# Kernel tuning notes

Hardware: AMD Instinct MI355X
Metric: run time of the kernel (lower is better)

Reference implementation:

```python
import jax, jax.numpy as jnp
import numpy as np

ALPHA = 0.2          # LeakyReLU negative slope
NEG_INF = -9e15      # mask value from the original code


def setup_inputs() -> dict:
    key = jax.random.key(0)
    k1, k2, k3, k4 = jax.random.split(key, 4)
    B, N, F_in, F_out = 8, 2048, 64, 64
    x = jax.random.normal(k1, (B, N, F_in), dtype=jnp.float32)
    adj = jax.random.randint(k2, (B, N, N), 0, 2, dtype=jnp.int32)
    W = jax.random.normal(k3, (F_in, F_out), dtype=jnp.float32)
    a = jax.random.normal(k4, (2 * F_out, 1), dtype=jnp.float32)
    return {"x": x, "adj": adj, "W": W, "a": a}


def reference(x, adj, W, a):
    # h: [B, N, F_out]
    h = jnp.matmul(x, W)
    F_out = W.shape[1]
    a1 = a[:F_out, 0]   # source half of attention vector
    a2 = a[F_out:, 0]   # target half
    # e_ij = leakyrelu(h_i . a1 + h_j . a2)  -- identical math to the
    # original cat([h_i, h_j]) @ a without materializing [B,N*N,2F].
    s1 = jnp.einsum('bnf,f->bn', h, a1)  # [B, N]
    s2 = jnp.einsum('bnf,f->bn', h, a2)  # [B, N]
    e = jax.nn.leaky_relu(s1[:, :, None] + s2[:, None, :], negative_slope=ALPHA)
    masked = jnp.where(adj > 0, e, NEG_INF)
    attention = jax.nn.softmax(masked, axis=2)  # [B, N, N]
    # dropout p=0.0 / eval mode -> identity
    h_prime = jnp.matmul(attention, h)          # [B, N, F_out]
    return jax.nn.elu(h_prime)                  # concat=True branch
```

## Files before the change

### kernel.cpp

```cpp
#include <hip/hip_runtime.h>
#include <cstdint>

#define LRELU_ALPHA 0.2f
#define NEG_INF -9000000000000000.0f
#define L2E 1.4426950408889634f

typedef __bf16 bf16x8 __attribute__((ext_vector_type(8)));
typedef float floatx4 __attribute__((ext_vector_type(4)));
typedef unsigned int uintx4 __attribute__((ext_vector_type(4)));

constexpr int Bb = 8, Nn = 2048, Ff = 64;
constexpr int TJ = 64;
constexpr int SEGW = 8;
constexpr int SLICE = Nn / SEGW;
constexpr int NT = SLICE / TJ;
constexpr int NROWS = Bb * Nn;
constexpr int MCH = Nn / 64;

__device__ __forceinline__ unsigned short f2bf(float f) {
    unsigned u = __builtin_bit_cast(unsigned, f);
    u = u + 0x7FFFu + ((u >> 16) & 1u);
    return (unsigned short)(u >> 16);
}

__device__ __forceinline__ unsigned cvt_pk_bf16(float lo, float hi) {
    unsigned r;
    asm("v_cvt_pk_bf16_f32 %0, %1, %2" : "=v"(r) : "v"(lo), "v"(hi));
    return r;
}

__global__ __launch_bounds__(256) void gat_prep(
    const float* __restrict__ x, const float* __restrict__ W, const float* __restrict__ a,
    unsigned short* __restrict__ hT, float* __restrict__ s1g, float* __restrict__ s2g)
{
    constexpr int STR2 = 36;
    __shared__ unsigned short hblk[64 * STR2];
    const int tid = threadIdx.x;
    const int blk = blockIdx.x;
    const int b  = blk >> 6;
    const int i0 = (blk & 63) * 32;
    const int w    = tid >> 6;
    const int lane = tid & 63;

    float wcol[64];
    #pragma unroll
    for (int k = 0; k < 64; ++k) wcol[k] = W[k * 64 + lane];
    const float a1 = a[lane], a2 = a[64 + lane];

    for (int r = 0; r < 8; ++r) {
        const int il = w * 8 + r;
        const int i  = i0 + il;
        const float* xrow = x + ((size_t)(b * Nn + i)) * 64;
        float h0 = 0.f, h1 = 0.f, h2 = 0.f, h3 = 0.f;
        #pragma unroll
        for (int k = 0; k < 64; k += 4) {
            h0 = fmaf(xrow[k],     wcol[k],     h0);
            h1 = fmaf(xrow[k + 1], wcol[k + 1], h1);
            h2 = fmaf(xrow[k + 2], wcol[k + 2], h2);
            h3 = fmaf(xrow[k + 3], wcol[k + 3], h3);
        }
        const float h = (h0 + h1) + (h2 + h3);
        float p1 = h * a1, p2 = h * a2;
        #pragma unroll
        for (int off = 32; off; off >>= 1) {
            p1 += __shfl_xor(p1, off);
            p2 += __shfl_xor(p2, off);
        }
        if (lane == 0) { s1g[b * Nn + i] = p1; s2g[b * Nn + i] = p2; }
        hblk[lane * STR2 + il] = f2bf(h);
    }
    __syncthreads();
    {
        const int f = tid >> 2, c = (tid & 3) * 8;
        uint4 v = *reinterpret_cast<const uint4*>(&hblk[f * STR2 + c]);
        *reinterpret_cast<uint4*>(hT + ((size_t)b * 64 + f) * Nn + i0 + c) = v;
    }
}

__global__ __launch_bounds__(512, 4) void gat_attn(
    const int* __restrict__ adj, const unsigned short* __restrict__ hT,
    const float* __restrict__ s1g, const float* __restrict__ s2g,
    float* __restrict__ out)
{
    __shared__ unsigned long long mk_lds[16][33];
    __shared__ float smax_lds[SEGW];
    __shared__ float O_lds[SEGW][16][65];
    __shared__ float l_lds[SEGW][16];

    const int tid  = threadIdx.x;
    const int blk  = blockIdx.x;
    const int b    = blk >> 7;
    const int i0   = (blk & 127) * 16;
    const int s    = tid >> 6;
    const int lane = tid & 63;
    const int fl   = lane & 15;
    const int q    = lane >> 4;

    {
        const float4 v = *reinterpret_cast<const float4*>(&s2g[b * Nn + s * SLICE + lane * 4]);
        float sm = fmaxf(fmaxf(v.x, v.y), fmaxf(v.z, v.w));
        #pragma unroll
        for (int off = 32; off; off >>= 1) sm = fmaxf(sm, __shfl_xor(sm, off));
        if (lane == 0) smax_lds[s] = sm;
    }

    #pragma unroll
    for (int rr = 0; rr < 2; ++rr) {
        const int rloc = s * 2 + rr;
        const int* ar = adj + ((size_t)(b * Nn + i0 + rloc)) * Nn;
        unsigned long long acc = 0;
        #pragma unroll
        for (int cb = 0; cb < MCH; ++cb) {
            const int v = ar[cb * 64 + lane];
            const unsigned long long mb = __ballot(v > 0);
            if (lane == cb) acc = mb;
        }
        if (lane < 32) mk_lds[rloc][lane] = acc;
    }

    const int i = i0 + fl;
    const float s1v = s1g[b * Nn + i];
    const unsigned short* hTb = hT + (size_t)b * 64 * Nn + s * SLICE;
    const float* s2b = s2g + b * Nn + s * SLICE;

    __syncthreads();

    float s2mx = smax_lds[0];
    #pragma unroll
    for (int k = 1; k < SEGW; ++k) s2mx = fmaxf(s2mx, smax_lds[k]);
    float mub = s1v + s2mx;
    mub = fmaxf(mub, LRELU_ALPHA * mub);
    const float ci = -mub * L2E;

    float l = 0.f;
    floatx4 C[4] = {};

    #pragma unroll
    for (int jt = 0; jt < NT; ++jt) {
        const int jloc = jt * TJ;

        const unsigned long long mk = mk_lds[fl][s * NT + jt];
        const float4 sA = *reinterpret_cast<const float4*>(&s2b[jloc + q * 8]);
        const float4 sB = *reinterpret_cast<const float4*>(&s2b[jloc + q * 8 + 4]);
        const float4 sC = *reinterpret_cast<const float4*>(&s2b[jloc + 32 + q * 8]);
        const float4 sD = *reinterpret_cast<const float4*>(&s2b[jloc + 32 + q * 8 + 4]);

        bf16x8 Bv[8];
        #pragma unroll
        for (int u = 0; u < 4; ++u) {
            Bv[2 * u] = *reinterpret_cast<const bf16x8*>(
                hTb + (size_t)(u * 16 + fl) * Nn + jloc + q * 8);
            Bv[2 * u + 1] = *reinterpret_cast<const bf16x8*>(
                hTb + (size_t)(u * 16 + fl) * Nn + jloc + 32 + q * 8);
        }

        const unsigned blo = ((unsigned)(mk >> (q * 8))) & 0xFFu;
        const unsigned bhi = ((unsigned)(mk >> (32 + q * 8))) & 0xFFu;

        float p[16];
        {
            const float s2v0[8] = { sA.x, sA.y, sA.z, sA.w, sB.x, sB.y, sB.z, sB.w };
            const float s2v1[8] = { sC.x, sC.y, sC.z, sC.w, sD.x, sD.y, sD.z, sD.w };
            #pragma unroll
            for (int jj = 0; jj < 8; ++jj) {
                float ev = s1v + s2v0[jj];
                ev = fmaxf(ev, LRELU_ALPHA * ev);
                const float t = exp2f(fmaf(ev, L2E, ci));
                p[jj] = (blo & (1u << jj)) ? t : 0.f;
                l += p[jj];
            }
            #pragma unroll
            for (int jj = 0; jj < 8; ++jj) {
                float ev = s1v + s2v1[jj];
                ev = fmaxf(ev, LRELU_ALPHA * ev);
                const float t = exp2f(fmaf(ev, L2E, ci));
                p[8 + jj] = (bhi & (1u << jj)) ? t : 0.f;
                l += p[8 + jj];
            }
        }

        uintx4 pa, pb;
        #pragma unroll
        for (int d = 0; d < 4; ++d) {
            pa[d] = cvt_pk_bf16(p[2 * d],     p[2 * d + 1]);
            pb[d] = cvt_pk_bf16(p[8 + 2 * d], p[8 + 2 * d + 1]);
        }
        const bf16x8 A0 = __builtin_bit_cast(bf16x8, pa);
        const bf16x8 A1 = __builtin_bit_cast(bf16x8, pb);

        __builtin_amdgcn_s_setprio(1);
        #pragma unroll
        for (int u = 0; u < 4; ++u) {
            C[u] = __builtin_amdgcn_mfma_f32_16x16x32_bf16(A0, Bv[2 * u],     C[u], 0, 0, 0);
            C[u] = __builtin_amdgcn_mfma_f32_16x16x32_bf16(A1, Bv[2 * u + 1], C[u], 0, 0, 0);
        }
        __builtin_amdgcn_s_setprio(0);
    }

    l += __shfl_xor(l, 16);
    l += __shfl_xor(l, 32);

    #pragma unroll
    for (int u = 0; u < 4; ++u)
        #pragma unroll
        for (int r = 0; r < 4; ++r)
            O_lds[s][q * 4 + r][u * 16 + fl] = C[u][r];
    if (q == 0) l_lds[s][fl] = l;
    __syncthreads();

    const int row = tid >> 5;
    const int f0  = (tid & 31) * 2;

    float lsum = 0.f, acc0 = 0.f, acc1 = 0.f;
    #pragma unroll
    for (int k = 0; k < SEGW; ++k) {
        lsum += l_lds[k][row];
        const float2 ov = *reinterpret_cast<const float2*>(&O_lds[k][row][f0]);
        acc0 += ov.x;
        acc1 += ov.y;
    }
    const float inv = 1.f / lsum;
    float v0 = acc0 * inv, v1 = acc1 * inv;
    v0 = (v0 > 0.f) ? v0 : (exp2f(v0 * L2E) - 1.f);
    v1 = (v1 > 0.f) ? v1 : (exp2f(v1 * L2E) - 1.f);
    float2 o2; o2.x = v0; o2.y = v1;
    *reinterpret_cast<float2*>(&out[((size_t)(b * Nn + i0 + row)) * 64 + f0]) = o2;
}

extern "C" void kernel_launch(void* const* d_in, const int* in_sizes, int n_in,
                              void* d_out, int out_size, void* d_ws, size_t ws_size,
                              hipStream_t stream) {
    const float* x   = (const float*)d_in[0];
    const int*   adj = (const int*)d_in[1];
    const float* W   = (const float*)d_in[2];
    const float* a   = (const float*)d_in[3];
    float* out = (float*)d_out;

    char* p = (char*)d_ws;
    unsigned short* hT = (unsigned short*)p;  p += (size_t)Bb * 64 * Nn * sizeof(unsigned short);
    float* s1 = (float*)p;                    p += (size_t)NROWS * sizeof(float);
    float* s2 = (float*)p;

    gat_prep<<<dim3(Bb * Nn / 32), dim3(256), 0, stream>>>(x, W, a, hT, s1, s2);
    gat_attn<<<dim3(NROWS / 16), dim3(512), 0, stream>>>(adj, hT, s1, s2, out);
}
```

Baseline: 237.3 us.

## Load adjacency with int4 per-wave slices and cache s2 in LDS

```diff
diff --git a/kernel.cpp b/kernel.cpp
--- a/kernel.cpp
+++ b/kernel.cpp
@@ -15,7 +15,6 @@
 constexpr int SLICE = Nn / SEGW;
 constexpr int NT = SLICE / TJ;
 constexpr int NROWS = Bb * Nn;
-constexpr int MCH = Nn / 64;
 
 __device__ __forceinline__ unsigned short f2bf(float f) {
     unsigned u = __builtin_bit_cast(unsigned, f);
@@ -82,10 +81,12 @@
     const float* __restrict__ s1g, const float* __restrict__ s2g,
     float* __restrict__ out)
 {
-    __shared__ unsigned long long mk_lds[16][33];
+    __shared__ unsigned long long mk_lds[SEGW][16][6];
+    __shared__ float s2_lds[Nn];
     __shared__ float smax_lds[SEGW];
     __shared__ float O_lds[SEGW][16][65];
     __shared__ float l_lds[SEGW][16];
+    __shared__ float lds_pad[2048];
 
     const int tid  = threadIdx.x;
     const int blk  = blockIdx.x;
@@ -98,30 +99,22 @@
 
     {
         const float4 v = *reinterpret_cast<const float4*>(&s2g[b * Nn + s * SLICE + lane * 4]);
+        *reinterpret_cast<float4*>(&s2_lds[s * SLICE + lane * 4]) = v;
         float sm = fmaxf(fmaxf(v.x, v.y), fmaxf(v.z, v.w));
         #pragma unroll
         for (int off = 32; off; off >>= 1) sm = fmaxf(sm, __shfl_xor(sm, off));
         if (lane == 0) smax_lds[s] = sm;
     }
 
-    #pragma unroll
-    for (int rr = 0; rr < 2; ++rr) {
-        const int rloc = s * 2 + rr;
-        const int* ar = adj + ((size_t)(b * Nn + i0 + rloc)) * Nn;
-        unsigned long long acc = 0;
-        #pragma unroll
-        for (int cb = 0; cb < MCH; ++cb) {
-            const int v = ar[cb * 64 + lane];
-            const unsigned long long mb = __ballot(v > 0);
-            if (lane == cb) acc = mb;
-        }
-        if (lane < 32) mk_lds[rloc][lane] = acc;
-    }
-
     const int i = i0 + fl;
     const float s1v = s1g[b * Nn + i];
-    const unsigned short* hTb = hT + (size_t)b * 64 * Nn + s * SLICE;
-    const float* s2b = s2g + b * Nn + s * SLICE;
+    if (blk == 0x7FFFFFFF) lds_pad[tid] = s1v;
+
+    const int4* adjb = reinterpret_cast<const int4*>(adj + (size_t)(b * Nn + i0) * Nn);
+    int4 va[16];
+    #pragma unroll
+    for (int r = 0; r < 16; ++r)
+        va[r] = adjb[(size_t)r * (Nn / 4) + s * 64 + lane];
 
     __syncthreads();
 
@@ -132,18 +125,35 @@
     mub = fmaxf(mub, LRELU_ALPHA * mub);
     const float ci = -mub * L2E;
 
+    {
+        unsigned long long acc = 0;
+        #pragma unroll
+        for (int r = 0; r < 16; ++r) {
+            const unsigned long long m0 = __ballot(va[r].x > 0);
+            const unsigned long long m1 = __ballot(va[r].y > 0);
+            const unsigned long long m2 = __ballot(va[r].z > 0);
+            const unsigned long long m3 = __ballot(va[r].w > 0);
+            const unsigned long long sel = (lane & 2) ? ((lane & 1) ? m3 : m2)
+                                                      : ((lane & 1) ? m1 : m0);
+            if ((lane >> 2) == r) acc = sel;
+        }
+        mk_lds[s][lane >> 2][lane & 3] = acc;
+    }
+    asm volatile("s_waitcnt lgkmcnt(0)" ::: "memory");
+    const unsigned long long w0 = mk_lds[s][fl][0];
+    const unsigned long long w1 = mk_lds[s][fl][1];
+    const unsigned long long w2 = mk_lds[s][fl][2];
+    const unsigned long long w3 = mk_lds[s][fl][3];
+
+    const unsigned short* hTb = hT + (size_t)b * 64 * Nn + s * SLICE;
+    const float* sl0 = &s2_lds[s * SLICE];
+
     float l = 0.f;
     floatx4 C[4] = {};
 
     #pragma unroll
     for (int jt = 0; jt < NT; ++jt) {
         const int jloc = jt * TJ;
-
-        const unsigned long long mk = mk_lds[fl][s * NT + jt];
-        const float4 sA = *reinterpret_cast<const float4*>(&s2b[jloc + q * 8]);
-        const float4 sB = *reinterpret_cast<const float4*>(&s2b[jloc + q * 8 + 4]);
-        const float4 sC = *reinterpret_cast<const float4*>(&s2b[jloc + 32 + q * 8]);
-        const float4 sD = *reinterpret_cast<const float4*>(&s2b[jloc + 32 + q * 8 + 4]);
 
         bf16x8 Bv[8];
         #pragma unroll
@@ -154,19 +164,29 @@
                 hTb + (size_t)(u * 16 + fl) * Nn + jloc + 32 + q * 8);
         }
 
-        const unsigned blo = ((unsigned)(mk >> (q * 8))) & 0xFFu;
-        const unsigned bhi = ((unsigned)(mk >> (32 + q * 8))) & 0xFFu;
+        const float4 sA = *reinterpret_cast<const float4*>(&sl0[jloc + q * 8]);
+        const float4 sB = *reinterpret_cast<const float4*>(&sl0[jloc + q * 8 + 4]);
+        const float4 sC = *reinterpret_cast<const float4*>(&sl0[jloc + 32 + q * 8]);
+        const float4 sD = *reinterpret_cast<const float4*>(&sl0[jloc + 32 + q * 8 + 4]);
+
+        const unsigned b0 = (unsigned)(jt * 16 + q * 2);
+        const unsigned t0w0 = (unsigned)(w0 >> b0),       t0w1 = (unsigned)(w1 >> b0);
+        const unsigned t0w2 = (unsigned)(w2 >> b0),       t0w3 = (unsigned)(w3 >> b0);
+        const unsigned t1w0 = (unsigned)(w0 >> (b0 + 8)), t1w1 = (unsigned)(w1 >> (b0 + 8));
+        const unsigned t1w2 = (unsigned)(w2 >> (b0 + 8)), t1w3 = (unsigned)(w3 >> (b0 + 8));
 
         float p[16];
         {
             const float s2v0[8] = { sA.x, sA.y, sA.z, sA.w, sB.x, sB.y, sB.z, sB.w };
             const float s2v1[8] = { sC.x, sC.y, sC.z, sC.w, sD.x, sD.y, sD.z, sD.w };
+            const unsigned tw0[4] = { t0w0, t0w1, t0w2, t0w3 };
+            const unsigned tw1[4] = { t1w0, t1w1, t1w2, t1w3 };
             #pragma unroll
             for (int jj = 0; jj < 8; ++jj) {
                 float ev = s1v + s2v0[jj];
                 ev = fmaxf(ev, LRELU_ALPHA * ev);
                 const float t = exp2f(fmaf(ev, L2E, ci));
-                p[jj] = (blo & (1u << jj)) ? t : 0.f;
+                p[jj] = ((tw0[jj & 3] >> (jj >> 2)) & 1u) ? t : 0.f;
                 l += p[jj];
             }
             #pragma unroll
@@ -174,7 +194,7 @@
                 float ev = s1v + s2v1[jj];
                 ev = fmaxf(ev, LRELU_ALPHA * ev);
                 const float t = exp2f(fmaf(ev, L2E, ci));
-                p[8 + jj] = (bhi & (1u << jj)) ? t : 0.f;
+                p[8 + jj] = ((tw1[jj & 3] >> (jj >> 2)) & 1u) ? t : 0.f;
                 l += p[8 + jj];
             }
         }
```

After: 230.4 us. -2.9%, faster.
